# Kernel optimization log

Measured on AMD Instinct MI355X. Metric: run time of the kernel, lower is better.

## Reference

```python
import jax, jax.numpy as jnp
import numpy as np


def _init_state(score_mat, key_blk, value_all):
    # score_mat: (B, Tn, Tt); key_blk: (B, Tn, Dk); value_all: (B, Tt, Dv)
    m = score_mat.max(axis=-1)                       # (B, Tn)
    e = jnp.exp(score_mat - m[..., None])            # (B, Tn, Tt)
    d = e.sum(axis=-1)                               # (B, Tn)
    norm = e / d[..., None]
    v_cache = jnp.einsum('bnt,btd->bnd', norm, value_all)
    return (m, d, key_blk, v_cache)


def _update_state(state, score_mat, value_blk):
    # Faithful to StreamingKVCacheState.get_updated_state (including its use of
    # the transposed new-query/old-key scores as old-query/new-key scores).
    m_old, d_old, k_cache, v_cache = state
    T_old = k_cache.shape[1]
    s_old = jnp.swapaxes(score_mat[:, :, :T_old], 1, 2)   # (B, T_old, T_new)
    new_m = jnp.maximum(m_old, s_old.max(axis=-1))        # (B, T_old)
    exp_neg_delta = jnp.exp(-(new_m - m_old))
    e = jnp.exp(s_old - new_m[..., None])                 # (B, T_old, T_new)
    new_d = d_old * exp_neg_delta + e.sum(axis=-1)
    ratio = new_d / d_old
    new_v = ratio[..., None] * v_cache + jnp.einsum('bnd,bon->bod', value_blk, e) / new_d[..., None]
    return (new_m, new_d, k_cache, new_v)


def _forward(x, Wq, bq, Wk, bk, Wv, bv, block_size):
    B, T, D = x.shape
    scale = D ** -0.5
    # torch.chunk(x, block_size, dim=1): split into block_size chunks
    blocks = jnp.split(x, block_size, axis=1)
    state = None
    for xb in blocks:
        q = xb @ Wq + bq
        k = xb @ Wk + bk
        v = xb @ Wv + bv
        if state is None:
            s = jnp.einsum('bqd,bkd->bqk', q, k) * scale
            state = _init_state(s, k, v)
        else:
            m, d, kc, vc = state
            k_cat = jnp.concatenate([kc, k], axis=1)
            v_cat = jnp.concatenate([vc, v], axis=1)   # note: v_cache, not raw values (faithful)
            s = jnp.einsum('bqd,bkd->bqk', q, k_cat) * scale
            upd = _update_state(state, s, v)
            new = _init_state(s, k, v_cat)
            state = tuple(jnp.concatenate([a, b], axis=1) for a, b in zip(upd, new))
    return state[3]  # final v_cache: (B, T, Dv)


def setup_inputs() -> dict:
    key = jax.random.key(0)
    ks = jax.random.split(key, 7)
    B, T, D = 8, 8192, 128
    w = D ** -0.5
    return {
        'x': jax.random.normal(ks[0], (B, T, D), jnp.float32),
        'Wq': jax.random.normal(ks[1], (D, D), jnp.float32) * w,
        'bq': jax.random.normal(ks[2], (D,), jnp.float32) * 0.01,
        'Wk': jax.random.normal(ks[3], (D, D), jnp.float32) * w,
        'bk': jax.random.normal(ks[4], (D,), jnp.float32) * 0.01,
        'Wv': jax.random.normal(ks[5], (D, D), jnp.float32) * w,
        'bv': jax.random.normal(ks[6], (D,), jnp.float32) * 0.01,
        'block_size': 8,
    }


def reference(x, Wq, bq, Wk, bk, Wv, bv, block_size):
    return _forward(x, Wq, bq, Wk, bk, Wv, bv, block_size)
```

## Files before the change

kernel.cpp:

```cpp
#include <hip/hip_runtime.h>

typedef __attribute__((ext_vector_type(8))) short bf16x8;
typedef __attribute__((ext_vector_type(4))) float f32x4;
typedef __attribute__((ext_vector_type(16))) float f32x16;
typedef unsigned short ushort_t;
typedef unsigned int uint32;

static constexpr int Bsz = 8;
static constexpr int T   = 8192;
static constexpr int Dd  = 128;
static constexpr int NB  = 8;
static constexpr int N   = T / NB;
static constexpr int Nk  = 64;
static constexpr int TPC = N / Nk;

__device__ __forceinline__ float bf2f(ushort_t u){
  return __uint_as_float(((uint32)u) << 16);
}
__device__ __forceinline__ ushort_t f2bf(float f){
  uint32 u = __float_as_uint(f);
  u += 0x7FFFu + ((u >> 16) & 1u);
  return (ushort_t)(u >> 16);
}
__device__ __forceinline__ uint32 cvtpk(float a, float b){
  uint32 r;
  asm("v_cvt_pk_bf16_f32 %0, %1, %2" : "=v"(r) : "v"(a), "v"(b));
  return r;
}
__device__ __forceinline__ float exp2v(float x){
  float r;
  asm("v_exp_f32 %0, %1" : "=v"(r) : "v"(x));
  return r;
}
typedef __attribute__((address_space(1))) const unsigned int guint;
typedef __attribute__((address_space(3))) unsigned int luint;
__device__ __forceinline__ void gl16(const void* g, void* l){
  __builtin_amdgcn_global_load_lds((guint*)g, (luint*)l, 16, 0, 0);
}

__global__ __launch_bounds__(256)
void proj_kernel(const float* __restrict__ X,
                 const float* __restrict__ Wq, const float* __restrict__ bq,
                 const float* __restrict__ Wk, const float* __restrict__ bk,
                 const float* __restrict__ Wv, const float* __restrict__ bv,
                 ushort_t* __restrict__ Qb, ushort_t* __restrict__ Kb,
                 ushort_t* __restrict__ VbT, float scale)
{
  __shared__ __align__(16) char smem[49152];
  short* Xt = (short*)smem;
  short* Wt = (short*)(smem + 16384);
  float* Brot = (float*)smem;

  const int which = blockIdx.y;
  const float* W   = (which == 0) ? Wq : (which == 1) ? Wk : Wv;
  const float* bia = (which == 0) ? bq : (which == 1) ? bk : bv;
  const float sc   = (which == 0) ? scale : 1.0f;

  const int tid  = threadIdx.x;
  const int wave = tid >> 6;
  const int lane = tid & 63;
  const int lg   = lane >> 4;
  const int lr   = lane & 15;
  const int row0 = blockIdx.x * 64;

  for (int c = tid; c < Dd*32; c += 256){
    int k  = c >> 5;
    int j0 = (c & 31) * 4;
    const float4 w = *reinterpret_cast<const float4*>(W + (size_t)k*Dd + j0);
    const float* wf = reinterpret_cast<const float*>(&w);
    #pragma unroll
    for (int e = 0; e < 4; e++){
      int jj = j0 + e;
      int inner = (k & 7) | (((k >> 3) ^ (jj & 7)) << 3);
      Wt[jj*Dd + inner] = (short)f2bf(wf[e]);
    }
  }
  for (int c = tid; c < 64*32; c += 256){
    int r  = c >> 5;
    int k0 = (c & 31) * 4;
    const float4 xv = *reinterpret_cast<const float4*>(X + (size_t)(row0 + r)*Dd + k0);
    const float* xf = reinterpret_cast<const float*>(&xv);
    int swz  = (k0 >> 3) ^ (r & 7);
    int base = r*Dd + swz*8 + (k0 & 7);
    #pragma unroll
    for (int e = 0; e < 4; e++) Xt[base + e] = (short)f2bf(xf[e]);
  }
  __syncthreads();

  f32x4 acc[8];
  #pragma unroll
  for (int nf = 0; nf < 8; nf++) acc[nf] = (f32x4){0.f,0.f,0.f,0.f};

  #pragma unroll
  for (int kk = 0; kk < 4; kk++){
    int arow = wave*16 + lr;
    int swz  = (lg + kk*4) ^ (lr & 7);
    bf16x8 a = *reinterpret_cast<const bf16x8*>(&Xt[arow*Dd + swz*8]);
    #pragma unroll
    for (int nf = 0; nf < 8; nf++){
      int col  = nf*16 + lr;
      bf16x8 b = *reinterpret_cast<const bf16x8*>(&Wt[col*Dd + swz*8]);
      acc[nf] = __builtin_amdgcn_mfma_f32_16x16x32_bf16(a, b, acc[nf], 0, 0, 0);
    }
  }

  if (which < 2){
    ushort_t* out = (which == 0) ? Qb : Kb;
    #pragma unroll
    for (int nf = 0; nf < 8; nf++){
      int col = nf*16 + lr;
      float bv_ = bia[col];
      #pragma unroll
      for (int r = 0; r < 4; r++){
        int grow = row0 + wave*16 + lg*4 + r;
        out[(size_t)grow*Dd + col] = f2bf((acc[nf][r] + bv_) * sc);
      }
    }
  } else {
    __syncthreads();
    #pragma unroll
    for (int nf = 0; nf < 8; nf++){
      int col = nf*16 + lr;
      float bv_ = bia[col];
      #pragma unroll
      for (int r = 0; r < 4; r++){
        int row_l = wave*16 + lg*4 + r;
        Brot[row_l*Dd + ((col + row_l) & 127)] = acc[nf][r] + bv_;
      }
    }
    __syncthreads();
    const int bb  = row0 >> 13;
    const int tq0 = row0 & (T - 1);
    const size_t vb = (size_t)bb * Dd * T;
    #pragma unroll 4
    for (int dd = 0; dd < 32; ++dd){
      int d = wave*32 + dd;
      float v = Brot[lane*Dd + ((d + lane) & 127)];
      VbT[vb + (size_t)d*T + tq0 + lane] = f2bf(v);
    }
  }
}

__global__ __launch_bounds__(256)
void attn_step(const ushort_t* __restrict__ Qb, const ushort_t* __restrict__ Kb,
               const ushort_t* __restrict__ VbT,
               const ushort_t* __restrict__ VcTr, ushort_t* __restrict__ VcTw,
               float* __restrict__ VcF, float* __restrict__ m_st, float* __restrict__ d_st,
               float* __restrict__ Pacc, float* __restrict__ Pm, float* __restrict__ Pmt,
               float* __restrict__ Pd, int iblk, int slog)
{
  __shared__ __align__(16) char smem[65536];

  const int tid  = threadIdx.x;
  const int wave = tid >> 6;
  const int lane = tid & 63;
  const int l31  = lane & 31;
  const int h    = lane >> 5;

  const int nwg = gridDim.x;
  const int bi  = (blockIdx.x & 7) * (nwg >> 3) + (blockIdx.x >> 3);

  const int slots = (iblk + 1) << slog;
  const int g0 = slots << 6;
  const bool is0 = (bi < g0);

  int b, qt, qrow0, t0, slot, ktiles;
  const ushort_t *qsrc, *ksrc, *vhi;

  if (is0){
    slot = bi >> 6;
    int sp = slot & ((1 << slog) - 1);
    int j  = slot >> slog;
    int rem = bi & 63;
    b = rem >> 3; qt = rem & 7;
    qrow0 = b*T + iblk*N + qt*128;
    ktiles = TPC >> slog;
    t0 = j*N + sp*(ktiles*Nk);
    qsrc = Qb; ksrc = Kb;
    vhi = (j < iblk) ? VcTr : VbT;
  } else {
    int bi2 = bi - g0;
    int per = 8 * iblk;
    b = bi2 / per;
    int rem = bi2 - b*per;
    int j = rem >> 3; qt = rem & 7;
    qrow0 = b*T + j*N + qt*128;
    ktiles = TPC;
    t0 = iblk*N;
    qsrc = Kb; ksrc = Qb;
    vhi = VbT;
    slot = 0;
  }
  const int krow0base = b*T + t0;
  const size_t vbase = (size_t)b * Dd * T;
  const ushort_t* vhiB = vhi + vbase;

  const ushort_t* kp = ksrc + (size_t)(krow0base + (tid >> 4))*Dd
                            + (((tid & 15) ^ ((tid >> 4) & 7)) << 3);
  const ushort_t* vp = vhiB + (size_t)(tid >> 3)*T + t0
                            + (((tid & 7) ^ ((tid >> 3) & 7)) << 3);

  auto STAGE = [&](const ushort_t* kpp, const ushort_t* vpp, int bufi){
    char* dstb = smem + bufi*32768 + (wave << 10);
    char* dstv = dstb + 16384;
    #pragma unroll
    for (int it = 0; it < 4; ++it){
      gl16(kpp + it*16*Dd, dstb + it*4096);
      gl16(vpp + (size_t)it*32*T, dstv + it*4096);
    }
  };

  bf16x8 qf[8];
  {
    const ushort_t* qp = qsrc + (size_t)(qrow0 + wave*32 + l31)*Dd + h*8;
    #pragma unroll
    for (int ks = 0; ks < 8; ++ks) qf[ks] = *reinterpret_cast<const bf16x8*>(qp + ks*16);
  }

  f32x16 o[4];
  #pragma unroll
  for (int db = 0; db < 4; ++db) o[db] = (f32x16)(0.0f);
  float m_rep  = 0.f;
  float tmax_h = -INFINITY;
  float d_half = 0.f;

  STAGE(kp, vp, 0);
  __syncthreads();
  int cur = 0;

  for (int kt = 0; kt < ktiles; ++kt){
    if (kt + 1 < ktiles){
      kp += 64*Dd; vp += 64;
      STAGE(kp, vp, cur ^ 1);
    }
    const short* Kt  = (const short*)(smem + cur*32768);
    const short* Vt0 = (const short*)(smem + cur*32768 + 16384);

    const float cini = (kt == 0) ? 0.f : -m_rep;
    f32x16 c0 = (f32x16)(cini), c1 = (f32x16)(cini);
    __builtin_amdgcn_s_setprio(1);
    #pragma unroll
    for (int ks = 0; ks < 8; ++ks){
      int swz = (2*ks + h) ^ (l31 & 7);
      bf16x8 ka = *reinterpret_cast<const bf16x8*>(&Kt[l31*Dd + swz*8]);
      bf16x8 kb = *reinterpret_cast<const bf16x8*>(&Kt[(32 + l31)*Dd + swz*8]);
      c0 = __builtin_amdgcn_mfma_f32_32x32x16_bf16(ka, qf[ks], c0, 0, 0, 0);
      c1 = __builtin_amdgcn_mfma_f32_32x32x16_bf16(kb, qf[ks], c1, 0, 0, 0);
    }
    __builtin_amdgcn_s_setprio(0);

    float tm = fmaxf(c0[0], c0[1]);
    #pragma unroll
    for (int r = 2; r < 16; r += 2) tm = fmaxf(tm, fmaxf(c0[r], c0[r+1]));
    #pragma unroll
    for (int r = 0; r < 16; r += 2) tm = fmaxf(tm, fmaxf(c1[r], c1[r+1]));

    float ps = 0.f;
    if (kt == 0){
      tm = fmaxf(tm, __shfl_xor(tm, 32));
      m_rep  = tm;
      tmax_h = tm;
      #pragma unroll
      for (int r = 0; r < 16; ++r){ c0[r] = exp2v(c0[r] - m_rep); ps += c0[r]; }
      #pragma unroll
      for (int r = 0; r < 16; ++r){ c1[r] = exp2v(c1[r] - m_rep); ps += c1[r]; }
    } else {
      tmax_h = fmaxf(tmax_h, tm + m_rep);
      #pragma unroll
      for (int r = 0; r < 16; ++r){ c0[r] = exp2v(c0[r]); ps += c0[r]; }
      #pragma unroll
      for (int r = 0; r < 16; ++r){ c1[r] = exp2v(c1[r]); ps += c1[r]; }
    }
    d_half += ps;

    uint32 w[16];
    #pragma unroll
    for (int q = 0; q < 8; ++q){
      w[q]     = cvtpk(c0[2*q], c0[2*q+1]);
      w[8 + q] = cvtpk(c1[2*q], c1[2*q+1]);
    }

    __builtin_amdgcn_s_setprio(1);
    #pragma unroll
    for (int s = 0; s < 4; ++s){
      uint32 x0 = (uint32)__shfl_xor((int)(h ? w[4*s]   : w[4*s+2]), 32);
      uint32 x1 = (uint32)__shfl_xor((int)(h ? w[4*s+1] : w[4*s+3]), 32);
      union { uint32 u[4]; bf16x8 v; } af;
      af.u[0] = h ? x0 : w[4*s];
      af.u[1] = h ? x1 : w[4*s+1];
      af.u[2] = h ? w[4*s+2] : x0;
      af.u[3] = h ? w[4*s+3] : x1;
      #pragma unroll
      for (int db = 0; db < 4; ++db){
        int swz = (2*s + h) ^ (l31 & 7);
        bf16x8 bv = *reinterpret_cast<const bf16x8*>(&Vt0[(db*32 + l31)*Nk + swz*8]);
        o[db] = __builtin_amdgcn_mfma_f32_32x32x16_bf16(af.v, bv, o[db], 0, 0, 0);
      }
    }
    __builtin_amdgcn_s_setprio(0);

    __syncthreads();
    cur ^= 1;
  }

  const float tm_true = fmaxf(tmax_h, __shfl_xor(tmax_h, 32));
  const float d_tot   = d_half + __shfl_xor(d_half, 32);

  if (is0){
    const int prow_base = b*1024 + qt*128 + wave*32;
    float* pa = Pacc + (size_t)slot*8192*Dd;
    #pragma unroll
    for (int r = 0; r < 16; ++r){
      int qloc = (r & 3) + 8*(r >> 2) + 4*h;
      float* row = pa + (size_t)(prow_base + qloc)*Dd + l31;
      #pragma unroll
      for (int db = 0; db < 4; ++db) row[db*32] = o[db][r];
    }
    if (lane < 32){
      Pm [slot*8192 + prow_base + l31] = m_rep;
      Pmt[slot*8192 + prow_base + l31] = tm_true;
      Pd [slot*8192 + prow_base + l31] = d_tot;
    }
  } else {
    const int growo = qrow0 + wave*32 + l31;
    float mo   = m_st[growo];
    float dold = d_st[growo];
    float mn   = fmaxf(mo, tm_true);
    float se   = exp2v(m_rep - mn);
    float nd   = dold * exp2v(mo - mn) + d_tot * se;
    float ratio = nd / dold;
    float accm  = se / nd;

    #pragma unroll
    for (int r = 0; r < 16; ++r){
      int rr = (r & 3) + 8*(r >> 2) + 4*h;
      float ratio_r = __shfl(ratio, rr);
      float accm_r  = __shfl(accm, rr);
      size_t base = (size_t)(qrow0 + wave*32 + rr)*Dd + l31;
      #pragma unroll
      for (int db = 0; db < 4; ++db){
        float v = ratio_r * VcF[base + db*32] + o[db][r] * accm_r;
        VcF[base + db*32] = v;
        o[db][r] = v;
      }
    }
    if (lane < 32){ m_st[growo] = mn; d_st[growo] = nd; }

    ushort_t* brot = (ushort_t*)smem + wave*4096;
    const int tabs = (qrow0 - b*T) + wave*32 + l31;
    #pragma unroll
    for (int r = 0; r < 16; ++r){
      int rr = (r & 3) + 8*(r >> 2) + 4*h;
      #pragma unroll
      for (int db = 0; db < 4; ++db){
        int d = db*32 + l31;
        brot[rr*128 + ((d + rr) & 127)] = f2bf(o[db][r]);
      }
    }
    #pragma unroll 4
    for (int dd = 0; dd < 64; ++dd){
      int d = dd*2 + h;
      VcTw[vbase + (size_t)d*T + tabs] = brot[l31*128 + ((d + l31) & 127)];
    }
  }
}

__global__ __launch_bounds__(256)
void merge_kernel(const float* __restrict__ Pacc, const float* __restrict__ Pm,
                  const float* __restrict__ Pmt, const float* __restrict__ Pd,
                  float* __restrict__ VcF, float* __restrict__ m_st, float* __restrict__ d_st,
                  ushort_t* __restrict__ VcTw, int slots, int iblk)
{
  __shared__ float Brot[64*Dd];
  const int bi = blockIdx.x;
  const int b = bi >> 4, qt = bi & 15;
  const int tid = threadIdx.x;
  const int lrow = tid >> 2, dq = tid & 3;
  const int prow = b*1024 + qt*64 + lrow;
  const int grow = b*T + iblk*N + qt*64 + lrow;

  float M = -INFINITY;
  for (int jj = 0; jj < slots; ++jj) M = fmaxf(M, Pmt[jj*8192 + prow]);

  float out[32];
  #pragma unroll
  for (int e = 0; e < 32; ++e) out[e] = 0.f;
  float D = 0.f;
  for (int jj = 0; jj < slots; ++jj){
    float wj = exp2v(Pm[jj*8192 + prow] - M);
    D += Pd[jj*8192 + prow] * wj;
    const float* pa = Pacc + ((size_t)jj*8192 + prow)*Dd + dq*32;
    #pragma unroll
    for (int e8 = 0; e8 < 8; ++e8){
      float4 v = *reinterpret_cast<const float4*>(pa + e8*4);
      out[e8*4+0] += v.x * wj;
      out[e8*4+1] += v.y * wj;
      out[e8*4+2] += v.z * wj;
      out[e8*4+3] += v.w * wj;
    }
  }
  float dinv = 1.f / D;
  #pragma unroll
  for (int e = 0; e < 32; ++e){
    int d = dq*32 + e;
    float v = out[e] * dinv;
    VcF[(size_t)grow*Dd + d] = v;
    Brot[lrow*Dd + ((d + lrow) & 127)] = v;
  }
  if (dq == 0){ m_st[grow] = M; d_st[grow] = D; }
  __syncthreads();

  const int wave = tid >> 6, lane = tid & 63;
  const int tq0 = iblk*N + qt*64;
  const size_t vb = (size_t)b * Dd * T;
  #pragma unroll 4
  for (int dd = 0; dd < 32; ++dd){
    int d = wave*32 + dd;
    float v = Brot[lane*Dd + ((d + lane) & 127)];
    VcTw[vb + (size_t)d*T + tq0 + lane] = f2bf(v);
  }
}

extern "C" void kernel_launch(void* const* d_in, const int* in_sizes, int n_in,
                              void* d_out, int out_size, void* d_ws, size_t ws_size,
                              hipStream_t stream)
{
  (void)in_sizes; (void)n_in; (void)out_size; (void)ws_size;

  const float* x  = (const float*)d_in[0];
  const float* Wq = (const float*)d_in[1];
  const float* bq = (const float*)d_in[2];
  const float* Wk = (const float*)d_in[3];
  const float* bk = (const float*)d_in[4];
  const float* Wv = (const float*)d_in[5];
  const float* bv = (const float*)d_in[6];

  float* VcF = (float*)d_out;

  const size_t nt = (size_t)Bsz * T;
  char* p = (char*)d_ws;
  auto alloc = [&](size_t bytes) -> void* {
    void* r = (void*)p;
    p += (bytes + 255) & ~(size_t)255;
    return r;
  };
  ushort_t* Qb   = (ushort_t*)alloc(nt * Dd * 2);
  ushort_t* Kb   = (ushort_t*)alloc(nt * Dd * 2);
  ushort_t* VbT  = (ushort_t*)alloc(nt * Dd * 2);
  ushort_t* VcT[2];
  for (int c = 0; c < 2; ++c)
    VcT[c] = (ushort_t*)alloc(nt * Dd * 2);
  float* m_st = (float*)alloc(nt * 4);
  float* d_st = (float*)alloc(nt * 4);
  float* Pacc = (float*)alloc((size_t)NB * 8192 * Dd * 4);
  float* Pm   = (float*)alloc((size_t)NB * 8192 * 4);
  float* Pmt  = (float*)alloc((size_t)NB * 8192 * 4);
  float* Pd   = (float*)alloc((size_t)NB * 8192 * 4);

  const float scale = 0.08838834764831845f * 1.4426950408889634f;
  dim3 blk(256);

  proj_kernel<<<dim3((unsigned)(nt / 64), 3), blk, 0, stream>>>(
      x, Wq, bq, Wk, bk, Wv, bv, Qb, Kb, VbT, scale);

  const int slogs[NB] = {3, 2, 1, 1, 0, 0, 0, 0};

  for (int i = 0; i < NB; ++i){
    const int wb = i & 1, rb = wb ^ 1;
    const int slog = slogs[i];
    const int slots = (i + 1) << slog;
    const int grid = 64 * slots + 64 * i;
    attn_step<<<grid, blk, 0, stream>>>(
        Qb, Kb, VbT, VcT[rb], VcT[wb],
        VcF, m_st, d_st, Pacc, Pm, Pmt, Pd, i, slog);
    merge_kernel<<<128, blk, 0, stream>>>(
        Pacc, Pm, Pmt, Pd, VcF, m_st, d_st, VcT[wb], slots, i);
  }
}
```

Baseline: 740.7 us.

## Halve key tile to 32 and use triple-buffered LDS pipeline with vmcnt waits

Shrinks the per-iteration key/value tile from 64 to 32 keys and switches the LDS staging from double to triple buffering, so loads run two tiles ahead. The full __syncthreads is replaced with explicit s_waitcnt vmcnt counts plus raw s_barrier, and the LDS swizzle patterns are adjusted for the new tile shapes. LDS use drops to 48KB, which may let more workgroups share a CU. In exchange there are twice as many iterations and barriers, each doing less MFMA work, and correctness depends on the hand-counted vmcnt values.

```diff
diff --git a/kernel.cpp b/kernel.cpp
--- a/kernel.cpp
+++ b/kernel.cpp
@@ -11,7 +11,7 @@
 static constexpr int Dd  = 128;
 static constexpr int NB  = 8;
 static constexpr int N   = T / NB;
-static constexpr int Nk  = 64;
+static constexpr int Nk  = 32;
 static constexpr int TPC = N / Nk;
 
 __device__ __forceinline__ float bf2f(ushort_t u){
@@ -149,7 +149,7 @@
                float* __restrict__ Pacc, float* __restrict__ Pm, float* __restrict__ Pmt,
                float* __restrict__ Pd, int iblk, int slog)
 {
-  __shared__ __align__(16) char smem[65536];
+  __shared__ __align__(16) char smem[49152];
 
   const int tid  = threadIdx.x;
   const int wave = tid >> 6;
@@ -196,17 +196,17 @@
   const ushort_t* vhiB = vhi + vbase;
 
   const ushort_t* kp = ksrc + (size_t)(krow0base + (tid >> 4))*Dd
-                            + (((tid & 15) ^ ((tid >> 4) & 7)) << 3);
-  const ushort_t* vp = vhiB + (size_t)(tid >> 3)*T + t0
-                            + (((tid & 7) ^ ((tid >> 3) & 7)) << 3);
+                            + (((tid & 15) ^ ((tid >> 4) & 15)) << 3);
+  const ushort_t* vp = vhiB + (size_t)(tid >> 2)*T + t0
+                            + (((tid & 3) ^ ((tid >> 2) & 3)) << 3);
 
   auto STAGE = [&](const ushort_t* kpp, const ushort_t* vpp, int bufi){
-    char* dstb = smem + bufi*32768 + (wave << 10);
-    char* dstv = dstb + 16384;
-    #pragma unroll
-    for (int it = 0; it < 4; ++it){
-      gl16(kpp + it*16*Dd, dstb + it*4096);
-      gl16(vpp + (size_t)it*32*T, dstv + it*4096);
+    char* dstk = smem + bufi*16384 + (wave << 10);
+    char* dstv = dstk + 8192;
+    #pragma unroll
+    for (int it = 0; it < 2; ++it){
+      gl16(kpp + it*16*Dd, dstk + it*4096);
+      gl16(vpp + (size_t)it*64*T, dstv + it*4096);
     }
   };
 
@@ -225,35 +225,40 @@
   float d_half = 0.f;
 
   STAGE(kp, vp, 0);
-  __syncthreads();
+  kp += Nk*Dd; vp += Nk;
+  STAGE(kp, vp, 1);
   int cur = 0;
 
   for (int kt = 0; kt < ktiles; ++kt){
-    if (kt + 1 < ktiles){
-      kp += 64*Dd; vp += 64;
-      STAGE(kp, vp, cur ^ 1);
-    }
-    const short* Kt  = (const short*)(smem + cur*32768);
-    const short* Vt0 = (const short*)(smem + cur*32768 + 16384);
-
-    const float cini = (kt == 0) ? 0.f : -m_rep;
-    f32x16 c0 = (f32x16)(cini), c1 = (f32x16)(cini);
+    if (kt + 2 < ktiles){
+      kp += Nk*Dd; vp += Nk;
+      int nb = cur + 2; if (nb >= 3) nb -= 3;
+      STAGE(kp, vp, nb);
+      asm volatile("s_waitcnt vmcnt(8)" ::: "memory");
+    } else if (kt + 1 < ktiles){
+      asm volatile("s_waitcnt vmcnt(4)" ::: "memory");
+    } else {
+      asm volatile("s_waitcnt vmcnt(0)" ::: "memory");
+    }
+    __builtin_amdgcn_s_barrier();
+    __builtin_amdgcn_sched_barrier(0);
+
+    const short* Kt = (const short*)(smem + cur*16384);
+    const short* Vt = (const short*)(smem + cur*16384 + 8192);
+
+    f32x16 c0 = (f32x16)((kt == 0) ? 0.f : -m_rep);
     __builtin_amdgcn_s_setprio(1);
     #pragma unroll
     for (int ks = 0; ks < 8; ++ks){
-      int swz = (2*ks + h) ^ (l31 & 7);
-      bf16x8 ka = *reinterpret_cast<const bf16x8*>(&Kt[l31*Dd + swz*8]);
-      bf16x8 kb = *reinterpret_cast<const bf16x8*>(&Kt[(32 + l31)*Dd + swz*8]);
+      int sl = (2*ks + h) ^ (l31 & 15);
+      bf16x8 ka = *reinterpret_cast<const bf16x8*>(&Kt[l31*128 + sl*8]);
       c0 = __builtin_amdgcn_mfma_f32_32x32x16_bf16(ka, qf[ks], c0, 0, 0, 0);
-      c1 = __builtin_amdgcn_mfma_f32_32x32x16_bf16(kb, qf[ks], c1, 0, 0, 0);
     }
     __builtin_amdgcn_s_setprio(0);
 
     float tm = fmaxf(c0[0], c0[1]);
     #pragma unroll
     for (int r = 2; r < 16; r += 2) tm = fmaxf(tm, fmaxf(c0[r], c0[r+1]));
-    #pragma unroll
-    for (int r = 0; r < 16; r += 2) tm = fmaxf(tm, fmaxf(c1[r], c1[r+1]));
 
     float ps = 0.f;
     if (kt == 0){
@@ -262,27 +267,20 @@
       tmax_h = tm;
       #pragma unroll
       for (int r = 0; r < 16; ++r){ c0[r] = exp2v(c0[r] - m_rep); ps += c0[r]; }
-      #pragma unroll
-      for (int r = 0; r < 16; ++r){ c1[r] = exp2v(c1[r] - m_rep); ps += c1[r]; }
     } else {
       tmax_h = fmaxf(tmax_h, tm + m_rep);
       #pragma unroll
       for (int r = 0; r < 16; ++r){ c0[r] = exp2v(c0[r]); ps += c0[r]; }
-      #pragma unroll
-      for (int r = 0; r < 16; ++r){ c1[r] = exp2v(c1[r]); ps += c1[r]; }
     }
     d_half += ps;
 
-    uint32 w[16];
-    #pragma unroll
-    for (int q = 0; q < 8; ++q){
-      w[q]     = cvtpk(c0[2*q], c0[2*q+1]);
-      w[8 + q] = cvtpk(c1[2*q], c1[2*q+1]);
-    }
+    uint32 w[8];
+    #pragma unroll
+    for (int q = 0; q < 8; ++q) w[q] = cvtpk(c0[2*q], c0[2*q+1]);
 
     __builtin_amdgcn_s_setprio(1);
     #pragma unroll
-    for (int s = 0; s < 4; ++s){
+    for (int s = 0; s < 2; ++s){
       uint32 x0 = (uint32)__shfl_xor((int)(h ? w[4*s]   : w[4*s+2]), 32);
       uint32 x1 = (uint32)__shfl_xor((int)(h ? w[4*s+1] : w[4*s+3]), 32);
       union { uint32 u[4]; bf16x8 v; } af;
@@ -292,15 +290,18 @@
       af.u[3] = h ? w[4*s+3] : x1;
       #pragma unroll
       for (int db = 0; db < 4; ++db){
-        int swz = (2*s + h) ^ (l31 & 7);
-        bf16x8 bv = *reinterpret_cast<const bf16x8*>(&Vt0[(db*32 + l31)*Nk + swz*8]);
+        int sl = (2*s + h) ^ (l31 & 3);
+        bf16x8 bv = *reinterpret_cast<const bf16x8*>(&Vt[(db*32 + l31)*32 + sl*8]);
         o[db] = __builtin_amdgcn_mfma_f32_32x32x16_bf16(af.v, bv, o[db], 0, 0, 0);
       }
     }
     __builtin_amdgcn_s_setprio(0);
 
-    __syncthreads();
-    cur ^= 1;
+    __builtin_amdgcn_sched_barrier(0);
+    asm volatile("" ::: "memory");
+    __builtin_amdgcn_s_barrier();
+    __builtin_amdgcn_sched_barrier(0);
+    cur = (cur + 1 == 3) ? 0 : cur + 1;
   }
 
   const float tm_true = fmaxf(tmax_h, __shfl_xor(tmax_h, 32));
```

Result: slower. 774.2 us (+4.5%).

## Load K/V fragments directly from global memory instead of LDS double-buffering

Applied to the files above, without the earlier changes.

Removes the global_load_lds double-buffered staging of K and V tiles into shared memory, along with its per-tile barriers. Each wave now reads its MFMA operands straight from global memory (served by L1/L2), and LDS shrinks to just the transpose scratch buffer. This cuts barrier and LDS traffic and may raise occupancy, but the four waves now redundantly fetch the same K/V data and lose the prefetch overlap, so global latency is exposed.

```diff
diff --git a/kernel.cpp b/kernel.cpp
--- a/kernel.cpp
+++ b/kernel.cpp
@@ -31,11 +31,6 @@
   float r;
   asm("v_exp_f32 %0, %1" : "=v"(r) : "v"(x));
   return r;
-}
-typedef __attribute__((address_space(1))) const unsigned int guint;
-typedef __attribute__((address_space(3))) unsigned int luint;
-__device__ __forceinline__ void gl16(const void* g, void* l){
-  __builtin_amdgcn_global_load_lds((guint*)g, (luint*)l, 16, 0, 0);
 }
 
 __global__ __launch_bounds__(256)
@@ -149,7 +144,7 @@
                float* __restrict__ Pacc, float* __restrict__ Pm, float* __restrict__ Pmt,
                float* __restrict__ Pd, int iblk, int slog)
 {
-  __shared__ __align__(16) char smem[65536];
+  __shared__ __align__(16) ushort_t brot_s[4][4096];
 
   const int tid  = threadIdx.x;
   const int wave = tid >> 6;
@@ -195,20 +190,9 @@
   const size_t vbase = (size_t)b * Dd * T;
   const ushort_t* vhiB = vhi + vbase;
 
-  const ushort_t* kp = ksrc + (size_t)(krow0base + (tid >> 4))*Dd
-                            + (((tid & 15) ^ ((tid >> 4) & 7)) << 3);
-  const ushort_t* vp = vhiB + (size_t)(tid >> 3)*T + t0
-                            + (((tid & 7) ^ ((tid >> 3) & 7)) << 3);
-
-  auto STAGE = [&](const ushort_t* kpp, const ushort_t* vpp, int bufi){
-    char* dstb = smem + bufi*32768 + (wave << 10);
-    char* dstv = dstb + 16384;
-    #pragma unroll
-    for (int it = 0; it < 4; ++it){
-      gl16(kpp + it*16*Dd, dstb + it*4096);
-      gl16(vpp + (size_t)it*32*T, dstv + it*4096);
-    }
-  };
+  const ushort_t* kbaseA = ksrc + (size_t)(krow0base + l31)*Dd + h*8;
+  const ushort_t* kbaseB = kbaseA + (size_t)32*Dd;
+  const ushort_t* vlane  = vhiB + (size_t)l31*T + t0 + h*8;
 
   bf16x8 qf[8];
   {
@@ -224,26 +208,17 @@
   float tmax_h = -INFINITY;
   float d_half = 0.f;
 
-  STAGE(kp, vp, 0);
-  __syncthreads();
-  int cur = 0;
-
   for (int kt = 0; kt < ktiles; ++kt){
-    if (kt + 1 < ktiles){
-      kp += 64*Dd; vp += 64;
-      STAGE(kp, vp, cur ^ 1);
-    }
-    const short* Kt  = (const short*)(smem + cur*32768);
-    const short* Vt0 = (const short*)(smem + cur*32768 + 16384);
+    const size_t offK = (size_t)kt * Nk * Dd;
+    const int    offV = kt * Nk;
 
     const float cini = (kt == 0) ? 0.f : -m_rep;
     f32x16 c0 = (f32x16)(cini), c1 = (f32x16)(cini);
     __builtin_amdgcn_s_setprio(1);
     #pragma unroll
     for (int ks = 0; ks < 8; ++ks){
-      int swz = (2*ks + h) ^ (l31 & 7);
-      bf16x8 ka = *reinterpret_cast<const bf16x8*>(&Kt[l31*Dd + swz*8]);
-      bf16x8 kb = *reinterpret_cast<const bf16x8*>(&Kt[(32 + l31)*Dd + swz*8]);
+      bf16x8 ka = *reinterpret_cast<const bf16x8*>(kbaseA + offK + ks*16);
+      bf16x8 kb = *reinterpret_cast<const bf16x8*>(kbaseB + offK + ks*16);
       c0 = __builtin_amdgcn_mfma_f32_32x32x16_bf16(ka, qf[ks], c0, 0, 0, 0);
       c1 = __builtin_amdgcn_mfma_f32_32x32x16_bf16(kb, qf[ks], c1, 0, 0, 0);
     }
@@ -292,15 +267,12 @@
       af.u[3] = h ? w[4*s+3] : x1;
       #pragma unroll
       for (int db = 0; db < 4; ++db){
-        int swz = (2*s + h) ^ (l31 & 7);
-        bf16x8 bv = *reinterpret_cast<const bf16x8*>(&Vt0[(db*32 + l31)*Nk + swz*8]);
+        bf16x8 bv = *reinterpret_cast<const bf16x8*>(
+            vlane + (size_t)(db*32)*T + offV + s*16);
         o[db] = __builtin_amdgcn_mfma_f32_32x32x16_bf16(af.v, bv, o[db], 0, 0, 0);
       }
     }
     __builtin_amdgcn_s_setprio(0);
-
-    __syncthreads();
-    cur ^= 1;
   }
 
   const float tm_true = fmaxf(tmax_h, __shfl_xor(tmax_h, 32));
@@ -346,7 +318,7 @@
     }
     if (lane < 32){ m_st[growo] = mn; d_st[growo] = nd; }
 
-    ushort_t* brot = (ushort_t*)smem + wave*4096;
+    ushort_t* brot = brot_s[wave];
     const int tabs = (qrow0 - b*T) + wave*32 + l31;
     #pragma unroll
     for (int r = 0; r < 16; ++r){
```

Result: slower. 1.633 ms (+120.5%).
